# Kernel tuning notes

Measured on AMD Instinct MI355X. Metric: run time of the kernel, lower is better.

Reference implementation:

```python
import jax, jax.numpy as jnp
import numpy as np
import math


def _alibi_slopes(n_heads):
    ratio = 2.0 ** (-8.0 / n_heads)
    return jnp.asarray([ratio ** i for i in range(1, n_heads + 1)], dtype=jnp.float32)


def setup_inputs() -> dict:
    key = jax.random.key(0)
    k1, k2, k3 = jax.random.split(key, 3)
    B, T, D = 2, 2048, 1024
    x = jax.random.normal(k1, (B, T, D), dtype=jnp.float32)
    W_qkv = jax.random.normal(k2, (3 * D, D), dtype=jnp.float32) * (1.0 / math.sqrt(D))
    W_out = jax.random.normal(k3, (D, D), dtype=jnp.float32) * (1.0 / math.sqrt(D))
    return {"x": x, "W_qkv": W_qkv, "W_out": W_out, "n_heads": 16}


def reference(x, W_qkv, W_out, n_heads):
    B, T, D = x.shape
    H = n_heads
    hd = D // H
    scale = 1.0 / math.sqrt(hd)

    # qkv projection: torch Linear computes x @ W.T ; W_qkv is [3D, D]
    qkv = jnp.einsum('btd,ed->bte', x, W_qkv)            # [B, T, 3D]
    qkv = qkv.reshape(B, T, 3, H, hd)
    q = jnp.transpose(qkv[:, :, 0], (0, 2, 1, 3))        # [B, H, T, hd]
    k = jnp.transpose(qkv[:, :, 1], (0, 2, 1, 3))
    v = jnp.transpose(qkv[:, :, 2], (0, 2, 1, 3))

    attn = jnp.einsum('bhqd,bhkd->bhqk', q, k) * scale   # [B, H, T, T]

    pos = jnp.arange(T)
    dist = jnp.abs(pos[None, :] - pos[:, None])          # [T, T]
    slopes = _alibi_slopes(H)                            # [H]
    attn = attn - slopes[None, :, None, None] * dist[None, None, :, :]

    causal = pos[None, :] > pos[:, None]                 # True above diagonal
    attn = jnp.where(causal[None, None, :, :], -jnp.inf, attn)
    attn = jax.nn.softmax(attn, axis=-1)

    out = jnp.einsum('bhqk,bhkd->bhqd', attn, v)         # [B, H, T, hd]
    out = jnp.transpose(out, (0, 2, 1, 3)).reshape(B, T, D)
    return jnp.einsum('btd,ed->bte', out, W_out)         # out projection
```

## Files before the change

### kernel.cpp

```cpp
#include <hip/hip_runtime.h>
#include <hip/hip_bf16.h>
#include <stdint.h>

typedef __attribute__((ext_vector_type(8))) short bf16x8;
typedef __attribute__((ext_vector_type(4))) short short4v;
typedef __attribute__((ext_vector_type(4))) float f32x4;

#define DEV static __device__ __forceinline__

DEV void load_lds16(const void* g, void* l) {
  __builtin_amdgcn_global_load_lds((const __attribute__((address_space(1))) char*)g,
                                   (__attribute__((address_space(3))) char*)l, 16, 0, 0);
}

DEV short f32_to_bf16_bits(float x) {
  union { __hip_bfloat16 h; short s; } u;
  u.h = __float2bfloat16(x);
  return u.s;
}
DEV float bf16_bits_to_f32(short s) {
  union { float f; unsigned u; } u;
  u.u = ((unsigned)(unsigned short)s) << 16;
  return u.f;
}

#define NX4 1048576
#define NQ4 786432
#define NW4 262144
__global__ __launch_bounds__(256) void conv_f32_bf16(const float4* __restrict__ x,
                                                     const float4* __restrict__ wq,
                                                     const float4* __restrict__ wo,
                                                     short4v* __restrict__ ox,
                                                     short4v* __restrict__ oq,
                                                     short4v* __restrict__ ow) {
  int i = blockIdx.x * 256 + threadIdx.x;
  const float4* src; short4v* dst; int j;
  if (i < NX4)            { src = x;  dst = ox; j = i; }
  else if (i < NX4 + NQ4) { src = wq; dst = oq; j = i - NX4; }
  else                    { src = wo; dst = ow; j = i - NX4 - NQ4; }
  float4 v = src[j];
  short4v s;
  s[0] = f32_to_bf16_bits(v.x); s[1] = f32_to_bf16_bits(v.y);
  s[2] = f32_to_bf16_bits(v.z); s[3] = f32_to_bf16_bits(v.w);
  dst[j] = s;
}

template<bool CF32>
__global__ __launch_bounds__(256) void gemm_bt(const __hip_bfloat16* __restrict__ A,
                                               const __hip_bfloat16* __restrict__ Bt,
                                               void* __restrict__ Cp,
                                               int M, int N, int K) {
  __shared__ short sA[128 * 64];
  __shared__ short sB[128 * 64];
  const int tid = threadIdx.x;
  const int lane = tid & 63;
  const int w = tid >> 6;
  const int wr = w >> 1, wc = w & 1;
  const int l15 = lane & 15, l4 = lane >> 4;
  const long m0 = (long)blockIdx.y * 128, n0 = (long)blockIdx.x * 128;

  f32x4 acc[4][4] = {};

  for (int k0 = 0; k0 < K; k0 += 64) {
    __syncthreads();
#pragma unroll
    for (int c = 0; c < 4; ++c) {
      int ci = c * 256 + tid;
      int row = ci >> 3;
      int sc = (ci & 7) ^ (row & 7);
      load_lds16(A + (m0 + row) * (long)K + k0 + sc * 8, (char*)sA + c * 4096 + w * 1024);
    }
#pragma unroll
    for (int c = 0; c < 4; ++c) {
      int ci = c * 256 + tid;
      int row = ci >> 3;
      int sc = (ci & 7) ^ (row & 7);
      load_lds16(Bt + (n0 + row) * (long)K + k0 + sc * 8, (char*)sB + c * 4096 + w * 1024);
    }
    __syncthreads();
#pragma unroll
    for (int ks = 0; ks < 2; ++ks) {
      bf16x8 av[4], bv[4];
#pragma unroll
      for (int i = 0; i < 4; ++i) {
        int row = wr * 64 + i * 16 + l15;
        int ch = (ks * 4 + l4) ^ (row & 7);
        av[i] = *(const bf16x8*)((const char*)sA + row * 128 + ch * 16);
      }
#pragma unroll
      for (int i = 0; i < 4; ++i) {
        int row = wc * 64 + i * 16 + l15;
        int ch = (ks * 4 + l4) ^ (row & 7);
        bv[i] = *(const bf16x8*)((const char*)sB + row * 128 + ch * 16);
      }
#pragma unroll
      for (int mi = 0; mi < 4; ++mi)
#pragma unroll
        for (int ni = 0; ni < 4; ++ni)
          acc[mi][ni] = __builtin_amdgcn_mfma_f32_16x16x32_bf16(av[mi], bv[ni], acc[mi][ni], 0, 0, 0);
    }
  }
#pragma unroll
  for (int mi = 0; mi < 4; ++mi)
#pragma unroll
    for (int r = 0; r < 4; ++r) {
      long row = m0 + wr * 64 + mi * 16 + l4 * 4 + r;
#pragma unroll
      for (int ni = 0; ni < 4; ++ni) {
        long col = n0 + wc * 64 + ni * 16 + l15;
        if constexpr (CF32)
          ((float*)Cp)[row * (long)N + col] = acc[mi][ni][r];
        else
          ((__hip_bfloat16*)Cp)[row * (long)N + col] = __float2bfloat16(acc[mi][ni][r]);
      }
    }
}

__global__ __launch_bounds__(256) void attn_fwd(const __hip_bfloat16* __restrict__ qkv,
                                                __hip_bfloat16* __restrict__ O) {
  constexpr int T = 2048;
  constexpr int LDQ = 3072;
  const int b = blockIdx.x >> 4;
  const int h = blockIdx.x & 15;
  const int q0 = (31 - (int)blockIdx.y) * 64;
  const int tid = threadIdx.x;
  const int lane = tid & 63;
  const int w = tid >> 6;
  const int l15 = lane & 15, l4 = lane >> 4;

  __shared__ short sK[64 * 64];
  __shared__ short sVT[64 * 72];
  __shared__ short sP[4][16 * 72];

  const float sl2 = exp2f(-0.5f * (float)(h + 1)) * 1.44269504f;
  const long base_bt = (long)b * T;

  bf16x8 qf[2];
#pragma unroll
  for (int ks = 0; ks < 2; ++ks) {
    long qrow = base_bt + q0 + w * 16 + l15;
    bf16x8 v = *(const bf16x8*)(qkv + qrow * LDQ + h * 64 + ks * 32 + l4 * 8);
#pragma unroll
    for (int j = 0; j < 8; ++j)
      v[j] = f32_to_bf16_bits(bf16_bits_to_f32(v[j]) * 0.18033688f);
    qf[ks] = v;
  }

  f32x4 oacc[4] = {};
  float mrun[4], lrun[4];
#pragma unroll
  for (int r = 0; r < 4; ++r) { mrun[r] = -1e30f; lrun[r] = 0.f; }

  for (int kv0 = 0; kv0 <= q0; kv0 += 64) {
    const bool masked = (kv0 == q0);
    __syncthreads();
#pragma unroll
    for (int c = 0; c < 2; ++c) {
      int ci = c * 256 + tid;
      int row = ci >> 3;
      int sc = (ci & 7) ^ (row & 7);
      load_lds16(qkv + (base_bt + kv0 + row) * LDQ + 1024 + h * 64 + sc * 8,
                 (char*)sK + c * 4096 + w * 1024);
    }
#pragma unroll
    for (int i = 0; i < 2; ++i) {
      int d0 = 8 * (w + 4 * i);
      bf16x8 v = *(const bf16x8*)(qkv + (base_bt + kv0 + lane) * LDQ + 2048 + h * 64 + d0);
#pragma unroll
      for (int j = 0; j < 8; ++j)
        sVT[(d0 + j) * 72 + lane] = v[j];
    }
    __syncthreads();

    f32x4 s[4] = {};
#pragma unroll
    for (int ks = 0; ks < 2; ++ks) {
      bf16x8 kf[4];
#pragma unroll
      for (int nf = 0; nf < 4; ++nf) {
        int row = nf * 16 + l15;
        int ch = (ks * 4 + l4) ^ (row & 7);
        kf[nf] = *(const bf16x8*)((const char*)sK + row * 128 + ch * 16);
      }
#pragma unroll
      for (int nf = 0; nf < 4; ++nf)
        s[nf] = __builtin_amdgcn_mfma_f32_16x16x32_bf16(qf[ks], kf[nf], s[nf], 0, 0, 0);
    }

    float al[4];
#pragma unroll
    for (int nf = 0; nf < 4; ++nf)
      al[nf] = sl2 * (float)(kv0 + nf * 16 + l15);

#pragma unroll
    for (int r = 0; r < 4; ++r) {
      float sv[4];
#pragma unroll
      for (int nf = 0; nf < 4; ++nf)
        sv[nf] = s[nf][r] + al[nf];
      if (masked) {
        int qloc = w * 16 + l4 * 4 + r;
#pragma unroll
        for (int nf = 0; nf < 4; ++nf)
          sv[nf] = (nf * 16 + l15 <= qloc) ? sv[nf] : -1e30f;
      }
      float mx = fmaxf(fmaxf(sv[0], sv[1]), fmaxf(sv[2], sv[3]));
#pragma unroll
      for (int off = 1; off < 16; off <<= 1)
        mx = fmaxf(mx, __shfl_xor(mx, off, 64));
      float mnew = fmaxf(mrun[r], mx);
      float f = exp2f(mrun[r] - mnew);
      mrun[r] = mnew;
      float p[4], sum;
#pragma unroll
      for (int nf = 0; nf < 4; ++nf)
        p[nf] = exp2f(sv[nf] - mnew);
      sum = (p[0] + p[1]) + (p[2] + p[3]);
      int qloc = l4 * 4 + r;
#pragma unroll
      for (int nf = 0; nf < 4; ++nf)
        sP[w][qloc * 72 + nf * 16 + l15] = f32_to_bf16_bits(p[nf]);
#pragma unroll
      for (int off = 1; off < 16; off <<= 1)
        sum += __shfl_xor(sum, off, 64);
      lrun[r] = lrun[r] * f + sum;
#pragma unroll
      for (int nd = 0; nd < 4; ++nd)
        oacc[nd][r] *= f;
    }

    asm volatile("s_waitcnt lgkmcnt(0)" ::: "memory");
    __builtin_amdgcn_sched_barrier(0);

#pragma unroll
    for (int ks = 0; ks < 2; ++ks) {
      bf16x8 pf = *(const bf16x8*)(sP[w] + l15 * 72 + ks * 32 + l4 * 8);
      bf16x8 vf[4];
#pragma unroll
      for (int nd = 0; nd < 4; ++nd)
        vf[nd] = *(const bf16x8*)(sVT + (nd * 16 + l15) * 72 + ks * 32 + l4 * 8);
#pragma unroll
      for (int nd = 0; nd < 4; ++nd)
        oacc[nd] = __builtin_amdgcn_mfma_f32_16x16x32_bf16(pf, vf[nd], oacc[nd], 0, 0, 0);
    }
  }

#pragma unroll
  for (int r = 0; r < 4; ++r) {
    long q = base_bt + q0 + w * 16 + l4 * 4 + r;
    float inv = 1.0f / lrun[r];
#pragma unroll
    for (int nd = 0; nd < 4; ++nd) {
      int d = nd * 16 + l15;
      O[q * 1024 + h * 64 + d] = __float2bfloat16(oacc[nd][r] * inv);
    }
  }
}

extern "C" void kernel_launch(void* const* d_in, const int* in_sizes, int n_in,
                              void* d_out, int out_size, void* d_ws, size_t ws_size,
                              hipStream_t stream) {
  const float* x    = (const float*)d_in[0];
  const float* Wqkv = (const float*)d_in[1];
  const float* Wout = (const float*)d_in[2];
  float* out = (float*)d_out;

  short* xb  = (short*)d_ws;
  short* wqb = xb + 4194304;
  short* wob = wqb + 3145728;
  short* qkv = wob + 1048576;
  short* attn = xb;

  dim3 blk(256);
  conv_f32_bf16<<<8192, blk, 0, stream>>>((const float4*)x, (const float4*)Wqkv,
                                          (const float4*)Wout, (short4v*)xb,
                                          (short4v*)wqb, (short4v*)wob);
  gemm_bt<false><<<dim3(24, 32), blk, 0, stream>>>((const __hip_bfloat16*)xb,
                                                   (const __hip_bfloat16*)wqb,
                                                   qkv, 4096, 3072, 1024);
  attn_fwd<<<dim3(32, 32), blk, 0, stream>>>((const __hip_bfloat16*)qkv,
                                             (__hip_bfloat16*)attn);
  gemm_bt<true><<<dim3(8, 32), blk, 0, stream>>>((const __hip_bfloat16*)attn,
                                                 (const __hip_bfloat16*)wob,
                                                 out, 4096, 1024, 1024);
}
```

Before: 212.9 us.

## Reverse KV order, lazy rescale, MFMA row sums, DPP max, smaller out-proj tiles

The attention loop now walks KV blocks from the diagonal backwards, so the running max is set early and the rescale of the accumulators runs only when some row max grows. Row sums are computed with an MFMA against a ones vector, using the bf16-rounded probabilities that also feed P·V. The row max reduction uses DPP intrinsics instead of shuffles. The output projection switches to a new 64x128-tile GEMM with twice as many blocks to improve occupancy on the small N=1024 problem. The new code carries extra branch and divergence logic, and the per-row max reduction now relies on the DPP control values being correct.

```diff
diff --git a/kernel.cpp b/kernel.cpp
--- a/kernel.cpp
+++ b/kernel.cpp
@@ -22,6 +22,21 @@
   union { float f; unsigned u; } u;
   u.u = ((unsigned)(unsigned short)s) << 16;
   return u.f;
+}
+
+template<int CTRL>
+DEV float dpp_fmax(float x) {
+  union { float f; int i; } u, v;
+  u.f = x;
+  v.i = __builtin_amdgcn_update_dpp(0, u.i, CTRL, 0xf, 0xf, true);
+  return fmaxf(x, v.f);
+}
+DEV float row16_max(float x) {
+  x = dpp_fmax<0xB1>(x);
+  x = dpp_fmax<0x4E>(x);
+  x = dpp_fmax<0x124>(x);
+  x = dpp_fmax<0x128>(x);
+  return x;
 }
 
 #define NX4 1048576
@@ -116,6 +131,72 @@
     }
 }
 
+__global__ __launch_bounds__(256) void gemm_bt64(const __hip_bfloat16* __restrict__ A,
+                                                 const __hip_bfloat16* __restrict__ Bt,
+                                                 float* __restrict__ C,
+                                                 int M, int N, int K) {
+  __shared__ short sA[64 * 64];
+  __shared__ short sB[128 * 64];
+  const int tid = threadIdx.x;
+  const int lane = tid & 63;
+  const int w = tid >> 6;
+  const int l15 = lane & 15, l4 = lane >> 4;
+  const long m0 = (long)blockIdx.y * 64, n0 = (long)blockIdx.x * 128;
+
+  f32x4 acc[4][2] = {};
+
+  for (int k0 = 0; k0 < K; k0 += 64) {
+    __syncthreads();
+#pragma unroll
+    for (int c = 0; c < 2; ++c) {
+      int ci = c * 256 + tid;
+      int row = ci >> 3;
+      int sc = (ci & 7) ^ (row & 7);
+      load_lds16(A + (m0 + row) * (long)K + k0 + sc * 8, (char*)sA + c * 4096 + w * 1024);
+    }
+#pragma unroll
+    for (int c = 0; c < 4; ++c) {
+      int ci = c * 256 + tid;
+      int row = ci >> 3;
+      int sc = (ci & 7) ^ (row & 7);
+      load_lds16(Bt + (n0 + row) * (long)K + k0 + sc * 8, (char*)sB + c * 4096 + w * 1024);
+    }
+    __syncthreads();
+#pragma unroll
+    for (int ks = 0; ks < 2; ++ks) {
+      bf16x8 av[4], bv[2];
+#pragma unroll
+      for (int i = 0; i < 4; ++i) {
+        int row = i * 16 + l15;
+        int ch = (ks * 4 + l4) ^ (row & 7);
+        av[i] = *(const bf16x8*)((const char*)sA + row * 128 + ch * 16);
+      }
+#pragma unroll
+      for (int i = 0; i < 2; ++i) {
+        int row = w * 32 + i * 16 + l15;
+        int ch = (ks * 4 + l4) ^ (row & 7);
+        bv[i] = *(const bf16x8*)((const char*)sB + row * 128 + ch * 16);
+      }
+#pragma unroll
+      for (int mi = 0; mi < 4; ++mi)
+#pragma unroll
+        for (int ni = 0; ni < 2; ++ni)
+          acc[mi][ni] = __builtin_amdgcn_mfma_f32_16x16x32_bf16(av[mi], bv[ni], acc[mi][ni], 0, 0, 0);
+    }
+  }
+#pragma unroll
+  for (int mi = 0; mi < 4; ++mi)
+#pragma unroll
+    for (int r = 0; r < 4; ++r) {
+      long row = m0 + mi * 16 + l4 * 4 + r;
+#pragma unroll
+      for (int ni = 0; ni < 2; ++ni) {
+        long col = n0 + w * 32 + ni * 16 + l15;
+        C[row * (long)N + col] = acc[mi][ni][r];
+      }
+    }
+}
+
 __global__ __launch_bounds__(256) void attn_fwd(const __hip_bfloat16* __restrict__ qkv,
                                                 __hip_bfloat16* __restrict__ O) {
   constexpr int T = 2048;
@@ -146,12 +227,17 @@
     qf[ks] = v;
   }
 
+  bf16x8 ones;
+#pragma unroll
+  for (int j = 0; j < 8; ++j) ones[j] = (short)0x3F80;
+
   f32x4 oacc[4] = {};
-  float mrun[4], lrun[4];
-#pragma unroll
-  for (int r = 0; r < 4; ++r) { mrun[r] = -1e30f; lrun[r] = 0.f; }
-
-  for (int kv0 = 0; kv0 <= q0; kv0 += 64) {
+  f32x4 lacc = {};
+  float mrun[4];
+#pragma unroll
+  for (int r = 0; r < 4; ++r) mrun[r] = -1e30f;
+
+  for (int kv0 = q0; kv0 >= 0; kv0 -= 64) {
     const bool masked = (kv0 == q0);
     __syncthreads();
 #pragma unroll
@@ -187,46 +273,45 @@
         s[nf] = __builtin_amdgcn_mfma_f32_16x16x32_bf16(qf[ks], kf[nf], s[nf], 0, 0, 0);
     }
 
-    float al[4];
-#pragma unroll
-    for (int nf = 0; nf < 4; ++nf)
-      al[nf] = sl2 * (float)(kv0 + nf * 16 + l15);
-
+    float mx[4];
 #pragma unroll
     for (int r = 0; r < 4; ++r) {
-      float sv[4];
-#pragma unroll
-      for (int nf = 0; nf < 4; ++nf)
-        sv[nf] = s[nf][r] + al[nf];
-      if (masked) {
-        int qloc = w * 16 + l4 * 4 + r;
-#pragma unroll
-        for (int nf = 0; nf < 4; ++nf)
-          sv[nf] = (nf * 16 + l15 <= qloc) ? sv[nf] : -1e30f;
-      }
-      float mx = fmaxf(fmaxf(sv[0], sv[1]), fmaxf(sv[2], sv[3]));
-#pragma unroll
-      for (int off = 1; off < 16; off <<= 1)
-        mx = fmaxf(mx, __shfl_xor(mx, off, 64));
-      float mnew = fmaxf(mrun[r], mx);
-      float f = exp2f(mrun[r] - mnew);
-      mrun[r] = mnew;
-      float p[4], sum;
-#pragma unroll
-      for (int nf = 0; nf < 4; ++nf)
-        p[nf] = exp2f(sv[nf] - mnew);
-      sum = (p[0] + p[1]) + (p[2] + p[3]);
+#pragma unroll
+      for (int nf = 0; nf < 4; ++nf) {
+        float val = s[nf][r] + sl2 * (float)(kv0 + nf * 16 + l15);
+        if (masked) {
+          int qloc = w * 16 + l4 * 4 + r;
+          val = (nf * 16 + l15 <= qloc) ? val : -1e30f;
+        }
+        s[nf][r] = val;
+      }
+      float m4 = fmaxf(fmaxf(s[0][r], s[1][r]), fmaxf(s[2][r], s[3][r]));
+      mx[r] = row16_max(m4);
+    }
+
+    bool grow = (mx[0] > mrun[0]) | (mx[1] > mrun[1]) |
+                (mx[2] > mrun[2]) | (mx[3] > mrun[3]);
+    if (__any(grow ? 1 : 0)) {
+#pragma unroll
+      for (int r = 0; r < 4; ++r) {
+        float mnew = fmaxf(mrun[r], mx[r]);
+        float f = exp2f(mrun[r] - mnew);
+        mrun[r] = mnew;
+        lacc[r] *= f;
+#pragma unroll
+        for (int nd = 0; nd < 4; ++nd)
+          oacc[nd][r] *= f;
+      }
+    }
+
+#pragma unroll
+    for (int r = 0; r < 4; ++r) {
       int qloc = l4 * 4 + r;
 #pragma unroll
-      for (int nf = 0; nf < 4; ++nf)
-        sP[w][qloc * 72 + nf * 16 + l15] = f32_to_bf16_bits(p[nf]);
-#pragma unroll
-      for (int off = 1; off < 16; off <<= 1)
-        sum += __shfl_xor(sum, off, 64);
-      lrun[r] = lrun[r] * f + sum;
-#pragma unroll
-      for (int nd = 0; nd < 4; ++nd)
-        oacc[nd][r] *= f;
+      for (int nf = 0; nf < 4; ++nf) {
+        float p = exp2f(s[nf][r] - mrun[r]);
+        sP[w][qloc * 72 + nf * 16 + l15] = f32_to_bf16_bits(p);
+      }
     }
 
     asm volatile("s_waitcnt lgkmcnt(0)" ::: "memory");
@@ -235,6 +320,7 @@
 #pragma unroll
     for (int ks = 0; ks < 2; ++ks) {
       bf16x8 pf = *(const bf16x8*)(sP[w] + l15 * 72 + ks * 32 + l4 * 8);
+      lacc = __builtin_amdgcn_mfma_f32_16x16x32_bf16(pf, ones, lacc, 0, 0, 0);
       bf16x8 vf[4];
 #pragma unroll
       for (int nd = 0; nd < 4; ++nd)
@@ -248,7 +334,7 @@
 #pragma unroll
   for (int r = 0; r < 4; ++r) {
     long q = base_bt + q0 + w * 16 + l4 * 4 + r;
-    float inv = 1.0f / lrun[r];
+    float inv = 1.0f / lacc[r];
 #pragma unroll
     for (int nd = 0; nd < 4; ++nd) {
       int d = nd * 16 + l15;
@@ -280,7 +366,7 @@
                                                    qkv, 4096, 3072, 1024);
   attn_fwd<<<dim3(32, 32), blk, 0, stream>>>((const __hip_bfloat16*)qkv,
                                              (__hip_bfloat16*)attn);
-  gemm_bt<true><<<dim3(8, 32), blk, 0, stream>>>((const __hip_bfloat16*)attn,
-                                                 (const __hip_bfloat16*)wob,
-                                                 out, 4096, 1024, 1024);
-}
+  gemm_bt64<<<dim3(8, 64), blk, 0, stream>>>((const __hip_bfloat16*)attn,
+                                             (const __hip_bfloat16*)wob,
+                                             out, 4096, 1024, 1024);
+}
```

Result: faster. 188.4 us (-11.5%).
